# Kernel optimization log

Hardware: AMD Instinct MI355X
Metric: run time of the kernel (lower is better)

Reference implementation:

```python
import jax, jax.numpy as jnp
import numpy as np

EPS = 1e-5

def _ln(x, g, b):
    m = jnp.mean(x, axis=-1, keepdims=True)
    v = jnp.mean((x - m) ** 2, axis=-1, keepdims=True)
    return (x - m) / jnp.sqrt(v + EPS) * g + b

B, SX, SY = 2, 2048, 2048
XD, YD, P, H, MULT = 1024, 1024, 64, 16, 4

def setup_inputs() -> dict:
    key = jax.random.key(0)
    ks = jax.random.split(key, 20)
    s = lambda fan: 1.0 / np.sqrt(fan)
    return {
        "x": jax.random.normal(ks[0], (B, SX, XD), jnp.float32),
        "y": jax.random.normal(ks[1], (B, SY, YD), jnp.float32),
        "gx_gamma": jnp.ones((XD,), jnp.float32),
        "gx_beta": jnp.zeros((XD,), jnp.float32),
        "gy_gamma": jnp.ones((YD,), jnp.float32),
        "gy_beta": jnp.zeros((YD,), jnp.float32),
        "Wq": jax.random.uniform(ks[2], (H, XD, P), jnp.float32, -s(XD), s(XD)),
        "bq": jax.random.uniform(ks[3], (H, P), jnp.float32, -s(XD), s(XD)),
        "Wk": jax.random.uniform(ks[4], (H, YD, P), jnp.float32, -s(YD), s(YD)),
        "bk": jax.random.uniform(ks[5], (H, P), jnp.float32, -s(YD), s(YD)),
        "Wv": jax.random.uniform(ks[6], (H, YD, P), jnp.float32, -s(YD), s(YD)),
        "bv": jax.random.uniform(ks[7], (H, P), jnp.float32, -s(YD), s(YD)),
        "Wo": jax.random.uniform(ks[8], (H * P, XD), jnp.float32, -s(H * P), s(H * P)),
        "bo": jax.random.uniform(ks[9], (XD,), jnp.float32, -s(H * P), s(H * P)),
        "gd_gamma": jnp.ones((XD,), jnp.float32),
        "gd_beta": jnp.zeros((XD,), jnp.float32),
        "W1": jax.random.uniform(ks[10], (XD, MULT * XD), jnp.float32, -s(XD), s(XD)),
        "b1": jax.random.uniform(ks[11], (MULT * XD,), jnp.float32, -s(XD), s(XD)),
        "W2": jax.random.uniform(ks[12], (MULT * XD, XD), jnp.float32, -s(MULT * XD), s(MULT * XD)),
        "b2": jax.random.uniform(ks[13], (XD,), jnp.float32, -s(MULT * XD), s(MULT * XD)),
        "mask": 1,
    }

def reference(x, y, gx_gamma, gx_beta, gy_gamma, gy_beta, Wq, bq, Wk, bk, Wv, bv,
              Wo, bo, gd_gamma, gd_beta, W1, b1, W2, b2, mask):
    xn = _ln(x, gx_gamma, gx_beta)
    yn = _ln(y, gy_gamma, gy_beta)
    # batched per-head projections: [B,S,D] x [H,D,P] -> [B,H,S,P]
    q = jnp.einsum('bsd,hdp->bhsp', xn, Wq) + bq[None, :, None, :]
    k = jnp.einsum('btd,hdp->bhtp', yn, Wk) + bk[None, :, None, :]
    v = jnp.einsum('btd,hdp->bhtp', yn, Wv) + bv[None, :, None, :]
    scores = jnp.einsum('bhsp,bhtp->bhst', q, k) * (1.0 / jnp.sqrt(jnp.float32(P)))
    attn = jax.nn.softmax(scores, axis=-1)
    if mask:
        # post-softmax strictly-upper-triangular mask (torch.triu diagonal=1)
        tri = jnp.triu(jnp.ones((SX, SY), attn.dtype), k=1)
        attn = attn * tri
    o = jnp.einsum('bhst,bhtp->bhsp', attn, v)          # [B,H,S,P]
    o = o.transpose(0, 2, 1, 3).reshape(B, SX, H * P)    # concat heads
    x2 = x + o @ Wo + bo
    h = jax.nn.gelu(_ln(x2, gd_gamma, gd_beta) @ W1 + b1, approximate=False)
    return x2 + h @ W2 + b2
```

## Files before the change

kernel.cpp:

```cpp
#include <hip/hip_runtime.h>
#include <hip/hip_bf16.h>
#include <math.h>

typedef __bf16 bf16_t;
typedef __bf16 bf16x8 __attribute__((ext_vector_type(8)));
typedef __bf16 bf16x4 __attribute__((ext_vector_type(4)));
typedef float f32x4 __attribute__((ext_vector_type(4)));

#define QSCALE 0.18033688011112042f

static __device__ __forceinline__ f32x4 mfma16(bf16x8 a, bf16x8 b, f32x4 c) {
  return __builtin_amdgcn_mfma_f32_16x16x32_bf16(a, b, c, 0, 0, 0);
}

static __device__ __forceinline__ float exp2_fast(float x) {
  float r;
  asm("v_exp_f32 %0, %1" : "=v"(r) : "v"(x));
  return r;
}

static __device__ __forceinline__ float gelu_f(float x) {
  const float u = x * (0.7978845608028654f + 0.03567740813636141f * x * x);
  const float a = fminf(u * 2.885390081777927f, 126.0f);
  const float e = exp2_fast(a);
  float r;
  asm("v_rcp_f32 %0, %1" : "=v"(r) : "v"(e + 1.0f));
  return x * e * r;
}

typedef __attribute__((address_space(1))) const void as1_void;
typedef __attribute__((address_space(3))) void as3_void;
static __device__ __forceinline__ void gload16(const void* g, void* s) {
  __builtin_amdgcn_global_load_lds((as1_void*)g, (as3_void*)s, 16, 0, 0);
}

static __device__ __forceinline__ long hmi(int row, int col) {
  return ((((long)(row >> 11) * 16 + (col >> 6)) * 2048) + (row & 2047)) * 64 + (col & 63);
}

__global__ __launch_bounds__(256) void prep_all(
    const float* __restrict__ Wq, const float* __restrict__ Wk, const float* __restrict__ Wv,
    const float* __restrict__ Wo, const float* __restrict__ W1, const float* __restrict__ W2,
    bf16_t* __restrict__ WqkvT, bf16_t* __restrict__ WoT, bf16_t* __restrict__ W1T,
    bf16_t* __restrict__ W2T, const float* __restrict__ x, const float* __restrict__ y,
    const float* __restrict__ gx, const float* __restrict__ bex, const float* __restrict__ gy,
    const float* __restrict__ bey, bf16_t* __restrict__ xn, bf16_t* __restrict__ yn) {
  const int bid = blockIdx.x;
  if (bid >= 3072) {
    const int lrow = bid - 3072;
    const float* in = lrow < 4096 ? x : y;
    const float* g = lrow < 4096 ? gx : gy;
    const float* be = lrow < 4096 ? bex : bey;
    bf16_t* out = lrow < 4096 ? xn : yn;
    const int row = lrow & 4095;
    const int t = threadIdx.x;
    const float4 xv = ((const float4*)(in + (long)row * 1024))[t];
    float s1 = xv.x + xv.y + xv.z + xv.w;
    float s2 = xv.x * xv.x + xv.y * xv.y + xv.z * xv.z + xv.w * xv.w;
#pragma unroll
    for (int m = 1; m < 64; m <<= 1) {
      s1 += __shfl_xor(s1, m);
      s2 += __shfl_xor(s2, m);
    }
    __shared__ float r1[4], r2[4];
    if ((t & 63) == 0) { r1[t >> 6] = s1; r2[t >> 6] = s2; }
    __syncthreads();
    s1 = r1[0] + r1[1] + r1[2] + r1[3];
    s2 = r2[0] + r2[1] + r2[2] + r2[3];
    const float mean = s1 * (1.0f / 1024.0f);
    float var = s2 * (1.0f / 1024.0f) - mean * mean;
    const float rstd = rsqrtf(fmaxf(var, 0.0f) + 1e-5f);
    const float4 gv = ((const float4*)g)[t];
    const float4 bv = ((const float4*)be)[t];
    bf16x4 o;
    o[0] = (bf16_t)((xv.x - mean) * rstd * gv.x + bv.x);
    o[1] = (bf16_t)((xv.y - mean) * rstd * gv.y + bv.y);
    o[2] = (bf16_t)((xv.z - mean) * rstd * gv.z + bv.z);
    o[3] = (bf16_t)((xv.w - mean) * rstd * gv.w + bv.w);
    *(bf16x4*)(out + (long)row * 1024 + t * 4) = o;
    return;
  }
  const float* inp;
  bf16_t* outp;
  int istride, ostride, i0, j0;
  if (bid < 768) {
    const int wsel = bid >> 8, rem = bid & 255;
    const int h = rem >> 4, xt = rem & 15;
    const float* W = wsel == 0 ? Wq : (wsel == 1 ? Wk : Wv);
    inp = W + h * 65536;
    outp = WqkvT + (long)wsel * 1048576 + h * 65536;
    istride = 64; ostride = 1024; i0 = xt * 64; j0 = 0;
  } else if (bid < 1024) {
    const int rem = bid - 768;
    inp = Wo; outp = WoT; istride = 1024; ostride = 1024;
    i0 = (rem & 15) * 64; j0 = (rem >> 4) * 64;
  } else if (bid < 2048) {
    const int rem = bid - 1024;
    inp = W1; outp = W1T; istride = 4096; ostride = 1024;
    i0 = (rem & 15) * 64; j0 = (rem >> 4) * 64;
  } else {
    const int rem = bid - 2048;
    inp = W2; outp = W2T; istride = 1024; ostride = 4096;
    i0 = (rem >> 4) * 64; j0 = (rem & 15) * 64;
  }
  __shared__ bf16_t tile[64][65];
  const int r = threadIdx.x >> 2, cs = (threadIdx.x & 3) * 16;
#pragma unroll
  for (int jj = 0; jj < 16; jj++)
    tile[cs + jj][r] = (bf16_t)inp[(long)(i0 + r) * istride + j0 + cs + jj];
  __syncthreads();
#pragma unroll
  for (int jj = 0; jj < 16; jj++)
    outp[(long)(j0 + r) * ostride + i0 + cs + jj] = tile[r][cs + jj];
}

__global__ __launch_bounds__(256) void ln_kernel(const float* __restrict__ in,
                                                 const float* __restrict__ g,
                                                 const float* __restrict__ be,
                                                 bf16_t* __restrict__ out) {
  const int row = blockIdx.x, t = threadIdx.x;
  const float4 xv = ((const float4*)(in + (long)row * 1024))[t];
  float s1 = xv.x + xv.y + xv.z + xv.w;
  float s2 = xv.x * xv.x + xv.y * xv.y + xv.z * xv.z + xv.w * xv.w;
#pragma unroll
  for (int m = 1; m < 64; m <<= 1) {
    s1 += __shfl_xor(s1, m);
    s2 += __shfl_xor(s2, m);
  }
  __shared__ float r1[4], r2[4];
  if ((t & 63) == 0) { r1[t >> 6] = s1; r2[t >> 6] = s2; }
  __syncthreads();
  s1 = r1[0] + r1[1] + r1[2] + r1[3];
  s2 = r2[0] + r2[1] + r2[2] + r2[3];
  const float mean = s1 * (1.0f / 1024.0f);
  float var = s2 * (1.0f / 1024.0f) - mean * mean;
  const float rstd = rsqrtf(fmaxf(var, 0.0f) + 1e-5f);
  const float4 gv = ((const float4*)g)[t];
  const float4 bv = ((const float4*)be)[t];
  bf16x4 o;
  o[0] = (bf16_t)((xv.x - mean) * rstd * gv.x + bv.x);
  o[1] = (bf16_t)((xv.y - mean) * rstd * gv.y + bv.y);
  o[2] = (bf16_t)((xv.z - mean) * rstd * gv.z + bv.z);
  o[3] = (bf16_t)((xv.w - mean) * rstd * gv.w + bv.w);
  *(bf16x4*)(out + (long)row * 1024 + t * 4) = o;
}

template <int EPI, int RW>
__global__ __launch_bounds__(512, 2) void gemm256(const bf16_t* __restrict__ A,
                                                  const bf16_t* __restrict__ Bt,
                                                  const float* __restrict__ bias,
                                                  void* __restrict__ Cout,
                                                  int M, int N, int K) {
  __shared__ bf16_t a_l[2][2][256 * 32];
  __shared__ bf16_t b_l[2][2][256 * 32];
  const int tid = threadIdx.x, l = tid & 63, wid = tid >> 6;
  const int wr = wid >> 2, wc = wid & 3;
  const int lr = l & 15, lg = l >> 4;
  const int nwg = gridDim.x * gridDim.y;
  const int orig = blockIdx.y * gridDim.x + blockIdx.x;
  const int cpx = nwg >> 3;
  const int xcd = orig & 7, ii = orig >> 3;
  const int rpr = gridDim.x / RW;
  const int bx = (xcd % rpr) * RW + (ii % RW);
  const int by = (xcd / rpr) * (cpx / RW) + (ii / RW);
  const int m0 = by * 256, n0 = bx * 256;
  const int nt = K >> 6;
  const int sr0 = tid >> 2, sr1 = 128 + (tid >> 2);
  const int sch2 = ((tid & 3) ^ ((tid >> 3) & 3)) * 8;
  const int sl0 = sr0 * 32 + (tid & 3) * 8;
  const int sl1 = sr1 * 32 + (tid & 3) * 8;
#define STG_A(bufi, kki, kcol)                                                  \
  do {                                                                          \
    gload16(A + (long)(m0 + sr0) * K + (kcol) + sch2, &a_l[bufi][kki][sl0]);    \
    gload16(A + (long)(m0 + sr1) * K + (kcol) + sch2, &a_l[bufi][kki][sl1]);    \
  } while (0)
#define STG_B(bufi, kki, kcol)                                                  \
  do {                                                                          \
    gload16(Bt + (long)(n0 + sr0) * K + (kcol) + sch2, &b_l[bufi][kki][sl0]);   \
    gload16(Bt + (long)(n0 + sr1) * K + (kcol) + sch2, &b_l[bufi][kki][sl1]);   \
  } while (0)
  const int ch = (lg ^ ((lr >> 1) & 3)) * 8;
  f32x4 acc[8][4] = {};
  bf16x8 af[8], bf2[2];
  STG_A(0, 0, 0); STG_B(0, 0, 0);
  STG_A(0, 1, 32); STG_B(0, 1, 32);
  STG_A(1, 0, 64); STG_B(1, 0, 64);
  asm volatile("s_waitcnt vmcnt(8)" ::: "memory");
  __builtin_amdgcn_s_barrier();
  for (int t = 0; t < nt; t++) {
    const int buf = t & 1, nbuf = buf ^ 1;
    const long kc = (long)t * 64;
#define RD_A(kki)                                                      \
  _Pragma("unroll") for (int m = 0; m < 8; m++) af[m] =                \
      *(const bf16x8*)&a_l[buf][kki][(wr * 128 + m * 16 + lr) * 32 + ch];
#define RD_B(kki, nh)                                                  \
  _Pragma("unroll") for (int j = 0; j < 2; j++) bf2[j] =               \
      *(const bf16x8*)&b_l[buf][kki][(wc * 64 + ((nh)*2 + j) * 16 + lr) * 32 + ch];
#define MM(nh)                                                         \
  __builtin_amdgcn_s_setprio(1);                                       \
  _Pragma("unroll") for (int m = 0; m < 8; m++) {                      \
    acc[m][(nh)*2 + 0] = mfma16(af[m], bf2[0], acc[m][(nh)*2 + 0]);    \
    acc[m][(nh)*2 + 1] = mfma16(af[m], bf2[1], acc[m][(nh)*2 + 1]);    \
  }                                                                    \
  __builtin_amdgcn_s_setprio(0);
    RD_A(0); RD_B(0, 0);
    if (t + 1 < nt) { STG_A(nbuf, 1, kc + 96); }
    __builtin_amdgcn_s_barrier();
    asm volatile("s_waitcnt lgkmcnt(0)" ::: "memory");
    __builtin_amdgcn_sched_barrier(0);
    MM(0);
    __builtin_amdgcn_s_barrier();
    RD_B(0, 1);
    if (t + 1 < nt) { STG_B(nbuf, 1, kc + 96); }
    if (t + 1 < nt) asm volatile("s_waitcnt vmcnt(8)" ::: "memory");
    else            asm volatile("s_waitcnt vmcnt(0)" ::: "memory");
    __builtin_amdgcn_s_barrier();
    asm volatile("s_waitcnt lgkmcnt(0)" ::: "memory");
    __builtin_amdgcn_sched_barrier(0);
    MM(1);
    __builtin_amdgcn_s_barrier();
    RD_A(1); RD_B(1, 0);
    if (t + 2 < nt) { STG_A(buf, 0, kc + 128); }
    __builtin_amdgcn_s_barrier();
    asm volatile("s_waitcnt lgkmcnt(0)" ::: "memory");
    __builtin_amdgcn_sched_barrier(0);
    MM(0);
    __builtin_amdgcn_s_barrier();
    RD_B(1, 1);
    if (t + 2 < nt) { STG_B(buf, 0, kc + 128); }
    if (t + 2 < nt)      asm volatile("s_waitcnt vmcnt(8)" ::: "memory");
    else if (t + 1 < nt) asm volatile("s_waitcnt vmcnt(4)" ::: "memory");
    __builtin_amdgcn_s_barrier();
    asm volatile("s_waitcnt lgkmcnt(0)" ::: "memory");
    __builtin_amdgcn_sched_barrier(0);
    MM(1);
    __builtin_amdgcn_s_barrier();
  }
#undef RD_A
#undef RD_B
#undef MM
#undef STG_A
#undef STG_B
#pragma unroll
  for (int m = 0; m < 8; m++)
#pragma unroll
    for (int n = 0; n < 4; n++) {
      const int row_b = m0 + wr * 128 + m * 16 + lg * 4;
      const int col = n0 + wc * 64 + n * 16 + lr;
      const float bia = bias[col];
#pragma unroll
      for (int r = 0; r < 4; r++) {
        const long idx = (long)(row_b + r) * N + col;
        if (EPI == 2) ((bf16_t*)Cout)[idx] = (bf16_t)gelu_f(acc[m][n][r] + bia);
      }
    }
}

template <int EPI, int BN, int RW>
__global__ __launch_bounds__(256) void gemm32(const bf16_t* __restrict__ A,
                                              const bf16_t* __restrict__ A2,
                                              const bf16_t* __restrict__ Bt,
                                              const float* __restrict__ bias,
                                              const float* __restrict__ biasB,
                                              const float* __restrict__ biasC,
                                              bf16_t* __restrict__ aux,
                                              void* __restrict__ Cout,
                                              int M, int N, int K) {
  constexpr int NF = BN / 32;
  constexpr int NBI = BN / 64;
  __shared__ bf16_t a_lds[3][128 * 32];
  __shared__ bf16_t b_lds[3][BN * 32];
  const int tid = threadIdx.x, l = tid & 63, w = tid >> 6;
  const int wr = w >> 1, wc = w & 1;
  const int nwg = gridDim.x * gridDim.y;
  const int orig = blockIdx.y * gridDim.x + blockIdx.x;
  const int cpx = nwg >> 3;
  const int xcd = orig & 7, ii = orig >> 3;
  const int rpr = gridDim.x / RW;
  const int bx = (xcd % rpr) * RW + (ii % RW);
  const int by = (xcd / rpr) * (cpx / RW) + (ii / RW);
  const int m0 = by * 128, n0 = bx * BN;
  const bf16_t* Ause = (EPI == 5 && n0 >= 1024) ? A2 : A;
  const int lr = l & 15, lg = l >> 4;
  long a_src[2];
  int a_dst[2];
#pragma unroll
  for (int i = 0; i < 2; i++) {
    const int row = i * 64 + (tid >> 2);
    const int sc = ((tid & 3) ^ ((row >> 1) & 3)) * 8;
    a_src[i] = (long)(m0 + row) * K + sc;
    a_dst[i] = (i * 64 + w * 16) * 32;
  }
  long b_src[NBI];
#pragma unroll
  for (int i = 0; i < NBI; i++) {
    const int row = i * 64 + (tid >> 2);
    const int sc = ((tid & 3) ^ ((row >> 1) & 3)) * 8;
    b_src[i] = (long)(n0 + row) * K + sc;
  }
  const int nk = K >> 5;
  f32x4 acc[4][NF] = {};
#pragma unroll
  for (int tt = 0; tt < 2; tt++) {
#pragma unroll
    for (int i = 0; i < 2; i++) gload16(Ause + a_src[i] + tt * 32, &a_lds[tt][a_dst[i]]);
#pragma unroll
    for (int i = 0; i < NBI; i++) gload16(Bt + b_src[i] + tt * 32, &b_lds[tt][a_dst[i]]);
  }
  int cu = 0;
  for (int t = 0; t < nk; t++) {
    if (t + 1 < nk) asm volatile("s_waitcnt vmcnt(4)" ::: "memory");
    else            asm volatile("s_waitcnt vmcnt(0)" ::: "memory");
    __builtin_amdgcn_s_barrier();
    __builtin_amdgcn_sched_barrier(0);
    if (t + 2 < nk) {
      const long k0 = (long)(t + 2) * 32;
      const int nb = cu >= 1 ? cu - 1 : 2;
#pragma unroll
      for (int i = 0; i < 2; i++) gload16(Ause + a_src[i] + k0, &a_lds[nb][a_dst[i]]);
#pragma unroll
      for (int i = 0; i < NBI; i++) gload16(Bt + b_src[i] + k0, &b_lds[nb][a_dst[i]]);
    }
    const char* ab = (const char*)&a_lds[cu][0];
    const char* bb = (const char*)&b_lds[cu][0];
    bf16x8 af[4], bfr[NF];
#pragma unroll
    for (int m = 0; m < 4; m++) {
      const int row = wr * 64 + m * 16 + lr;
      af[m] = *(const bf16x8*)(ab + row * 64 + 16 * (lg ^ ((row >> 1) & 3)));
    }
#pragma unroll
    for (int n = 0; n < NF; n++) {
      const int row = wc * (BN / 2) + n * 16 + lr;
      bfr[n] = *(const bf16x8*)(bb + row * 64 + 16 * (lg ^ ((row >> 1) & 3)));
    }
    __builtin_amdgcn_s_setprio(1);
#pragma unroll
    for (int m = 0; m < 4; m++)
#pragma unroll
      for (int n = 0; n < NF; n++) acc[m][n] = mfma16(af[m], bfr[n], acc[m][n]);
    __builtin_amdgcn_s_setprio(0);
    cu = cu < 2 ? cu + 1 : 0;
  }
#pragma unroll
  for (int m = 0; m < 4; m++)
#pragma unroll
    for (int n = 0; n < NF; n++) {
      const int row_b = m0 + wr * 64 + m * 16 + (l >> 4) * 4;
      const int col = n0 + wc * (BN / 2) + n * 16 + lr;
      if (EPI == 5) {
        if (col < 1024) {
          const float bia = bias[col];
#pragma unroll
          for (int r = 0; r < 4; r++)
            ((bf16_t*)Cout)[hmi(row_b + r, col)] = (bf16_t)((acc[m][n][r] + bia) * QSCALE);
        } else if (col < 2048) {
          const float bia = biasB[col - 1024];
#pragma unroll
          for (int r = 0; r < 4; r++)
            ((bf16_t*)Cout + 4194304)[hmi(row_b + r, col - 1024)] =
                (bf16_t)(acc[m][n][r] + bia);
        } else {
          const int vcol = col - 2048;
          const float bia = biasC[vcol];
          bf16x4 vv;
#pragma unroll
          for (int r = 0; r < 4; r++) vv[r] = (bf16_t)(acc[m][n][r] + bia);
          const int bb2 = row_b >> 11, tt = row_b & 2047;
          *(bf16x4*)&aux[(((long)(bb2 << 4) + (vcol >> 6)) * 64 + (vcol & 63)) * 2048 + tt] = vv;
        }
      }
    }
}

template <int EPI, int BN>
__global__ __launch_bounds__(256) void gemm64(const bf16_t* __restrict__ A,
                                              const bf16_t* __restrict__ Bt,
                                              const float* __restrict__ bias,
                                              const float* __restrict__ res,
                                              void* __restrict__ Cout,
                                              int M, int N, int K) {
  constexpr int NF = BN / 32;
  constexpr int NBI = BN / 32;
  __shared__ bf16_t a_lds[2][128 * 64];
  __shared__ bf16_t b_lds[2][BN * 64];
  const int tid = threadIdx.x, l = tid & 63, w = tid >> 6;
  const int wr = w >> 1, wc = w & 1;
  const int nwg = gridDim.x * gridDim.y;
  const int orig = blockIdx.y * gridDim.x + blockIdx.x;
  const int lid = (orig & 7) * (nwg >> 3) + (orig >> 3);
  const int bx = lid % gridDim.x, by = lid / gridDim.x;
  const int m0 = by * 128, n0 = bx * BN;
  const int lr = l & 15, lg = l >> 4;
  long a_src[4];
  int ldst[4];
#pragma unroll
  for (int i = 0; i < 4; i++) {
    const int row = i * 32 + w * 8 + (l >> 3);
    const int sc = ((l & 7) ^ (row & 7)) * 8;
    a_src[i] = (long)(m0 + row) * K + sc;
    ldst[i] = (i * 32 + w * 8) * 64;
  }
  long b_src[NBI];
#pragma unroll
  for (int i = 0; i < NBI; i++) {
    const int row = i * 32 + w * 8 + (l >> 3);
    const int sc = ((l & 7) ^ (row & 7)) * 8;
    b_src[i] = (long)(n0 + row) * K + sc;
  }
  const int nk = K >> 6;
  f32x4 acc[4][NF] = {};
#pragma unroll
  for (int i = 0; i < 4; i++) gload16(A + a_src[i], &a_lds[0][ldst[i]]);
#pragma unroll
  for (int i = 0; i < NBI; i++) gload16(Bt + b_src[i], &b_lds[0][ldst[i]]);
  __syncthreads();
  const int sw = (lr & 7) << 4;
  int cur = 0;
  for (int t = 0; t < nk; t++) {
    if (t + 1 < nk) {
      const long k0 = (long)(t + 1) * 64;
#pragma unroll
      for (int i = 0; i < 4; i++) gload16(A + a_src[i] + k0, &a_lds[cur ^ 1][ldst[i]]);
#pragma unroll
      for (int i = 0; i < NBI; i++) gload16(Bt + b_src[i] + k0, &b_lds[cur ^ 1][ldst[i]]);
    }
    const char* ab = (const char*)&a_lds[cur][0];
    const char* bb = (const char*)&b_lds[cur][0];
    bf16x8 af[4][2], bfr[NF][2];
#pragma unroll
    for (int m = 0; m < 4; m++) {
      const int rb = (wr * 64 + m * 16 + lr) * 128;
      af[m][0] = *(const bf16x8*)(ab + rb + ((16 * lg) ^ sw));
      af[m][1] = *(const bf16x8*)(ab + rb + ((16 * lg + 64) ^ sw));
    }
#pragma unroll
    for (int n = 0; n < NF; n++) {
      const int rb = (wc * (BN / 2) + n * 16 + lr) * 128;
      bfr[n][0] = *(const bf16x8*)(bb + rb + ((16 * lg) ^ sw));
      bfr[n][1] = *(const bf16x8*)(bb + rb + ((16 * lg + 64) ^ sw));
    }
    __builtin_amdgcn_s_setprio(1);
#pragma unroll
    for (int kk = 0; kk < 2; kk++)
#pragma unroll
      for (int m = 0; m < 4; m++)
#pragma unroll
        for (int n = 0; n < NF; n++)
          acc[m][n] = mfma16(af[m][kk], bfr[n][kk], acc[m][n]);
    __builtin_amdgcn_s_setprio(0);
    __syncthreads();
    cur ^= 1;
  }
#pragma unroll
  for (int m = 0; m < 4; m++)
#pragma unroll
    for (int n = 0; n < NF; n++) {
      const int row_b = m0 + wr * 64 + m * 16 + (l >> 4) * 4;
      const int col = n0 + wc * (BN / 2) + n * 16 + lr;
      const float bia = bias[col];
#pragma unroll
      for (int r = 0; r < 4; r++) {
        const long idx = (long)(row_b + r) * N + col;
        ((float*)Cout)[idx] = acc[m][n][r] + bia + res[idx];
      }
    }
}

__global__ __launch_bounds__(256) void attn_kernel(const bf16_t* __restrict__ qhm,
                                                   const bf16_t* __restrict__ khm,
                                                   const bf16_t* __restrict__ vtg,
                                                   bf16_t* __restrict__ og,
                                                   const int* __restrict__ maskp) {
  const int T = 2048, HP = 1024;
  __shared__ bf16_t k_lds[2][64 * 64];
  __shared__ bf16_t vt_lds[2][64 * 64];
  __shared__ bf16_t p_lds[4 * 32 * 72];
  const int bh = blockIdx.x, b = bh >> 4, h = bh & 15;
  const int q0 = blockIdx.y * 128;
  const int tid = threadIdx.x, l = tid & 63, w = tid >> 6;
  const int lr = l & 15, lg = l >> 4, lg4 = lg * 4;
  const int srow0 = q0 + w * 32 + lr;
  const bf16_t* kbase = khm + (long)bh * T * 64;
  const bf16_t* vbase = vtg + (long)bh * 64 * T;
  bf16x8 qf[2][2];
#pragma unroll
  for (int g = 0; g < 2; g++) {
    const bf16_t* qr = qhm + ((long)bh * 2048 + srow0 + g * 16) * 64 + lg * 8;
    qf[g][0] = *(const bf16x8*)qr;
    qf[g][1] = *(const bf16x8*)(qr + 32);
  }
  bf16_t* pl = &p_lds[w * 32 * 72];
  float lpart[2] = {0.0f, 0.0f};
  f32x4 oat[4][2] = {};

  const int swz = (lr & 7) << 4;
  const int fo0 = lr * 128 + ((16 * lg) ^ swz);
  const int fo1 = lr * 128 + ((64 + 16 * lg) ^ swz);

  const bool do_mask = (maskp[0] != 0);
  const int nM = do_mask ? (q0 >> 6) : 0;
  const int nt = T >> 6;

  const int sch = l & 7, srow8 = l >> 3;
  int cur = 0;
  {
    const bool needV = (nM == 0);
#pragma unroll
    for (int i = 0; i < 2; i++) {
      const int row = (i * 4 + w) * 8 + srow8;
      const int sc = (sch ^ (row & 7)) * 8;
      gload16(kbase + (long)row * 64 + sc, &k_lds[0][(i * 4 + w) * 512]);
      if (needV) gload16(vbase + (long)row * 2048 + 0 + sc, &vt_lds[0][(i * 4 + w) * 512]);
    }
  }
  __syncthreads();

  for (int t = 0; t < nt; t++) {
    const int t0 = t << 6;
    const int mode = (t < nM) ? 0 : ((do_mask && t < nM + 2) ? 1 : 2);
    if (t + 1 < nt) {
      const int t1 = (t + 1) << 6;
      const bool needV = (t + 1) >= nM;
#pragma unroll
      for (int i = 0; i < 2; i++) {
        const int row = (i * 4 + w) * 8 + srow8;
        const int sc = (sch ^ (row & 7)) * 8;
        gload16(kbase + (long)(t1 + row) * 64 + sc, &k_lds[cur ^ 1][(i * 4 + w) * 512]);
        if (needV)
          gload16(vbase + (long)row * 2048 + t1 + sc, &vt_lds[cur ^ 1][(i * 4 + w) * 512]);
      }
    }
    const char* kb = (const char*)&k_lds[cur][0];
    f32x4 sacc[4][2];
    __builtin_amdgcn_s_setprio(1);
#pragma unroll
    for (int n = 0; n < 4; n++) {
      bf16x8 kf0 = *(const bf16x8*)(kb + n * 2048 + fo0);
      bf16x8 kf1 = *(const bf16x8*)(kb + n * 2048 + fo1);
#pragma unroll
      for (int g = 0; g < 2; g++) {
        f32x4 z = {0.0f, 0.0f, 0.0f, 0.0f};
        z = mfma16(kf0, qf[g][0], z);
        sacc[n][g] = mfma16(kf1, qf[g][1], z);
      }
    }
    __builtin_amdgcn_s_setprio(0);
    float pv[2][4][4];
#pragma unroll
    for (int g = 0; g < 2; g++) {
      float psn[4];
#pragma unroll
      for (int n = 0; n < 4; n++) {
        pv[g][n][0] = exp2_fast(sacc[n][g][0]);
        pv[g][n][1] = exp2_fast(sacc[n][g][1]);
        pv[g][n][2] = exp2_fast(sacc[n][g][2]);
        pv[g][n][3] = exp2_fast(sacc[n][g][3]);
        psn[n] = (pv[g][n][0] + pv[g][n][1]) + (pv[g][n][2] + pv[g][n][3]);
      }
      lpart[g] += (psn[0] + psn[1]) + (psn[2] + psn[3]);
    }
    if (mode > 0) {
#pragma unroll
      for (int g = 0; g < 2; g++)
#pragma unroll
        for (int n = 0; n < 4; n++) {
          bf16x4 pk;
#pragma unroll
          for (int r = 0; r < 4; r++) {
            float v = pv[g][n][r];
            if (mode == 1 && (t0 + n * 16 + lg4 + r) <= srow0 + g * 16) v = 0.0f;
            pk[r] = (bf16_t)v;
          }
          *(bf16x4*)&pl[(g * 16 + lr) * 72 + n * 16 + lg4] = pk;
        }
      const char* vtb = (const char*)&vt_lds[cur][0];
      __builtin_amdgcn_s_setprio(1);
#pragma unroll
      for (int kk = 0; kk < 2; kk++) {
        bf16x8 pb0 = *(bf16x8*)&pl[lr * 72 + kk * 32 + lg * 8];
        bf16x8 pb1 = *(bf16x8*)&pl[(16 + lr) * 72 + kk * 32 + lg * 8];
        const int fkk = lr * 128 + ((kk * 64 + 16 * lg) ^ swz);
#pragma unroll
        for (int np = 0; np < 4; np++) {
          bf16x8 vtf = *(const bf16x8*)(vtb + np * 2048 + fkk);
          oat[np][0] = mfma16(vtf, pb0, oat[np][0]);
          oat[np][1] = mfma16(vtf, pb1, oat[np][1]);
        }
      }
      __builtin_amdgcn_s_setprio(0);
    }
    __syncthreads();
    cur ^= 1;
  }
  float inv[2];
#pragma unroll
  for (int g = 0; g < 2; g++) {
    float lsum = lpart[g];
    lsum += __shfl_xor(lsum, 16);
    lsum += __shfl_xor(lsum, 32);
    inv[g] = 1.0f / lsum;
  }
#pragma unroll
  for (int g = 0; g < 2; g++)
#pragma unroll
    for (int np = 0; np < 4; np++) {
      bf16x4 o4;
#pragma unroll
      for (int r = 0; r < 4; r++) o4[r] = (bf16_t)(oat[np][g][r] * inv[g]);
      *(bf16x4*)&pl[(g * 16 + lr) * 72 + np * 16 + lg4] = o4;
    }
  const int es = l >> 2, ec = (l & 3) * 16;
#pragma unroll
  for (int g = 0; g < 2; g++) {
    bf16x8 o0 = *(bf16x8*)&pl[(g * 16 + es) * 72 + ec];
    bf16x8 o1 = *(bf16x8*)&pl[(g * 16 + es) * 72 + ec + 8];
    bf16_t* orow = og + (long)(b * 2048 + q0 + w * 32 + g * 16 + es) * HP + h * 64 + ec;
    *(bf16x8*)&orow[0] = o0;
    *(bf16x8*)&orow[8] = o1;
  }
}

extern "C" void kernel_launch(void* const* d_in, const int* in_sizes, int n_in,
                              void* d_out, int out_size, void* d_ws, size_t ws_size,
                              hipStream_t stream) {
  const float* x = (const float*)d_in[0];
  const float* y = (const float*)d_in[1];
  const float* gxg = (const float*)d_in[2];
  const float* gxb = (const float*)d_in[3];
  const float* gyg = (const float*)d_in[4];
  const float* gyb = (const float*)d_in[5];
  const float* Wq = (const float*)d_in[6];
  const float* bq = (const float*)d_in[7];
  const float* Wk = (const float*)d_in[8];
  const float* bk = (const float*)d_in[9];
  const float* Wv = (const float*)d_in[10];
  const float* bv = (const float*)d_in[11];
  const float* Wo = (const float*)d_in[12];
  const float* bo = (const float*)d_in[13];
  const float* gdg = (const float*)d_in[14];
  const float* gdb = (const float*)d_in[15];
  const float* W1 = (const float*)d_in[16];
  const float* b1 = (const float*)d_in[17];
  const float* W2 = (const float*)d_in[18];
  const float* b2 = (const float*)d_in[19];
  const int* maskp = (const int*)d_in[20];
  float* out = (float*)d_out;

  char* ws = (char*)d_ws;
  const long MB = 1024 * 1024;
  bf16_t* xn = (bf16_t*)(ws + 0);
  bf16_t* yn = (bf16_t*)(ws + 8 * MB);
  bf16_t* WqkvT = (bf16_t*)(ws + 16 * MB);
  bf16_t* WoT = (bf16_t*)(ws + 22 * MB);
  bf16_t* W1T = (bf16_t*)(ws + 24 * MB);
  bf16_t* W2T = (bf16_t*)(ws + 32 * MB);
  bf16_t* qhm = (bf16_t*)(ws + 40 * MB);
  bf16_t* vTb = (bf16_t*)(ws + 64 * MB);
  bf16_t* ob = (bf16_t*)(ws + 0);
  bf16_t* xd = (bf16_t*)(ws + 8 * MB);
  bf16_t* hb = (bf16_t*)(ws + 40 * MB);
  bf16_t* khm = qhm + 4194304;

  prep_all<<<11264, 256, 0, stream>>>(Wq, Wk, Wv, Wo, W1, W2, WqkvT, WoT, W1T, W2T, x, y, gxg,
                                      gxb, gyg, gyb, xn, yn);
  gemm32<5, 128, 12><<<dim3(24, 32), 256, 0, stream>>>(xn, yn, WqkvT, bq, bk, bv, vTb, qhm,
                                                       4096, 3072, 1024);
  attn_kernel<<<dim3(32, 16), 256, 0, stream>>>(qhm, khm, vTb, ob, maskp);
  gemm64<1, 64><<<dim3(16, 32), 256, 0, stream>>>(ob, WoT, bo, x, out, 4096, 1024, 1024);
  ln_kernel<<<4096, 256, 0, stream>>>(out, gdg, gdb, xd);
  gemm256<2, 4><<<dim3(16, 16), 512, 0, stream>>>(xd, W1T, b1, hb, 4096, 4096, 1024);
  gemm64<1, 64><<<dim3(16, 32), 256, 0, stream>>>(hb, W2T, b2, out, out, 4096, 1024, 4096);
}
```

Baseline: 229.8 us.

## Split-K the W2 GEMM on the 256-tile kernel with a separate reduction

The final FFN down-projection (K=4096) moves from the 64-wide GEMM to the 256x256 tile GEMM with split-K by 4. The grid is 4x16x4 workgroups, and each writes a bf16 partial tile into workspace. A new reduce kernel sums the four partials, adds bias b2 and accumulates into the residual output. The intent is to use the more efficient large-tile MFMA kernel while keeping enough workgroups to fill the device. The cost is extra partial write/read traffic, an added launch, and bf16 rounding of the partial sums.

```diff
diff --git a/kernel.cpp b/kernel.cpp
--- a/kernel.cpp
+++ b/kernel.cpp
@@ -145,6 +145,28 @@
   *(bf16x4*)(out + (long)row * 1024 + t * 4) = o;
 }
 
+__global__ __launch_bounds__(256) void reduce_w2(const bf16_t* __restrict__ part,
+                                                 const float* __restrict__ b2,
+                                                 float* __restrict__ out) {
+  const long base = (long)blockIdx.x * 1024 + threadIdx.x * 4;
+  float4 o = *(float4*)(out + base);
+  const float4 bb = ((const float4*)b2)[threadIdx.x];
+  float s0 = 0.0f, s1 = 0.0f, s2 = 0.0f, s3 = 0.0f;
+#pragma unroll
+  for (int s = 0; s < 4; s++) {
+    bf16x4 p = *(const bf16x4*)(part + ((long)s << 22) + base);
+    s0 += (float)p[0];
+    s1 += (float)p[1];
+    s2 += (float)p[2];
+    s3 += (float)p[3];
+  }
+  o.x += s0 + bb.x;
+  o.y += s1 + bb.y;
+  o.z += s2 + bb.z;
+  o.w += s3 + bb.w;
+  *(float4*)(out + base) = o;
+}
+
 template <int EPI, int RW>
 __global__ __launch_bounds__(512, 2) void gemm256(const bf16_t* __restrict__ A,
                                                   const bf16_t* __restrict__ Bt,
@@ -156,15 +178,24 @@
   const int tid = threadIdx.x, l = tid & 63, wid = tid >> 6;
   const int wr = wid >> 2, wc = wid & 3;
   const int lr = l & 15, lg = l >> 4;
-  const int nwg = gridDim.x * gridDim.y;
-  const int orig = blockIdx.y * gridDim.x + blockIdx.x;
-  const int cpx = nwg >> 3;
-  const int xcd = orig & 7, ii = orig >> 3;
-  const int rpr = gridDim.x / RW;
-  const int bx = (xcd % rpr) * RW + (ii % RW);
-  const int by = (xcd / rpr) * (cpx / RW) + (ii / RW);
+  const int nwg = gridDim.x * gridDim.y * gridDim.z;
+  const int orig = (blockIdx.z * gridDim.y + blockIdx.y) * gridDim.x + blockIdx.x;
+  int bx, by, ks = 0;
+  if (EPI == 7) {
+    const int lid = (orig & 7) * (nwg >> 3) + (orig >> 3);
+    bx = lid % gridDim.x;
+    by = (lid / gridDim.x) % gridDim.y;
+    ks = lid / (gridDim.x * gridDim.y);
+  } else {
+    const int cpx = nwg >> 3;
+    const int xcd = orig & 7, ii = orig >> 3;
+    const int rpr = gridDim.x / RW;
+    bx = (xcd % rpr) * RW + (ii % RW);
+    by = (xcd / rpr) * (cpx / RW) + (ii / RW);
+  }
   const int m0 = by * 256, n0 = bx * 256;
-  const int nt = K >> 6;
+  const long kbase = (EPI == 7) ? (long)ks << 10 : 0;
+  const int nt = (EPI == 7) ? 16 : (K >> 6);
   const int sr0 = tid >> 2, sr1 = 128 + (tid >> 2);
   const int sch2 = ((tid & 3) ^ ((tid >> 3) & 3)) * 8;
   const int sl0 = sr0 * 32 + (tid & 3) * 8;
@@ -182,14 +213,14 @@
   const int ch = (lg ^ ((lr >> 1) & 3)) * 8;
   f32x4 acc[8][4] = {};
   bf16x8 af[8], bf2[2];
-  STG_A(0, 0, 0); STG_B(0, 0, 0);
-  STG_A(0, 1, 32); STG_B(0, 1, 32);
-  STG_A(1, 0, 64); STG_B(1, 0, 64);
+  STG_A(0, 0, kbase + 0); STG_B(0, 0, kbase + 0);
+  STG_A(0, 1, kbase + 32); STG_B(0, 1, kbase + 32);
+  STG_A(1, 0, kbase + 64); STG_B(1, 0, kbase + 64);
   asm volatile("s_waitcnt vmcnt(8)" ::: "memory");
   __builtin_amdgcn_s_barrier();
   for (int t = 0; t < nt; t++) {
     const int buf = t & 1, nbuf = buf ^ 1;
-    const long kc = (long)t * 64;
+    const long kc = kbase + (long)t * 64;
 #define RD_A(kki)                                                      \
   _Pragma("unroll") for (int m = 0; m < 8; m++) af[m] =                \
       *(const bf16x8*)&a_l[buf][kki][(wr * 128 + m * 16 + lr) * 32 + ch];
@@ -247,11 +278,18 @@
     for (int n = 0; n < 4; n++) {
       const int row_b = m0 + wr * 128 + m * 16 + lg * 4;
       const int col = n0 + wc * 64 + n * 16 + lr;
-      const float bia = bias[col];
-#pragma unroll
-      for (int r = 0; r < 4; r++) {
-        const long idx = (long)(row_b + r) * N + col;
-        if (EPI == 2) ((bf16_t*)Cout)[idx] = (bf16_t)gelu_f(acc[m][n][r] + bia);
+      if (EPI == 2) {
+        const float bia = bias[col];
+#pragma unroll
+        for (int r = 0; r < 4; r++) {
+          const long idx = (long)(row_b + r) * N + col;
+          ((bf16_t*)Cout)[idx] = (bf16_t)gelu_f(acc[m][n][r] + bia);
+        }
+      } else if (EPI == 7) {
+        bf16_t* part = (bf16_t*)Cout + ((long)ks << 22);
+#pragma unroll
+        for (int r = 0; r < 4; r++)
+          part[(long)(row_b + r) * N + col] = (bf16_t)acc[m][n][r];
       }
     }
 }
@@ -660,6 +698,7 @@
   bf16_t* ob = (bf16_t*)(ws + 0);
   bf16_t* xd = (bf16_t*)(ws + 8 * MB);
   bf16_t* hb = (bf16_t*)(ws + 40 * MB);
+  bf16_t* w2part = (bf16_t*)(ws + 0);
   bf16_t* khm = qhm + 4194304;
 
   prep_all<<<11264, 256, 0, stream>>>(Wq, Wk, Wv, Wo, W1, W2, WqkvT, WoT, W1T, W2T, x, y, gxg,
@@ -670,5 +709,6 @@
   gemm64<1, 64><<<dim3(16, 32), 256, 0, stream>>>(ob, WoT, bo, x, out, 4096, 1024, 1024);
   ln_kernel<<<4096, 256, 0, stream>>>(out, gdg, gdb, xd);
   gemm256<2, 4><<<dim3(16, 16), 512, 0, stream>>>(xd, W1T, b1, hb, 4096, 4096, 1024);
-  gemm64<1, 64><<<dim3(16, 32), 256, 0, stream>>>(hb, W2T, b2, out, out, 4096, 1024, 4096);
-}
+  gemm256<7, 4><<<dim3(4, 16, 4), 512, 0, stream>>>(hb, W2T, nullptr, w2part, 4096, 1024, 4096);
+  reduce_w2<<<4096, 256, 0, stream>>>(w2part, b2, out);
+}
```

Result: faster. 224.8 us, median of 2 (-2.2%).
